# Kernel tuning notes

Measured on AMD Instinct MI355X. Metric: run time of the kernel, lower is better.

## Reference

```python
import jax, jax.numpy as jnp
import numpy as np

K = 3          # conv kernel size
PW = 4         # parallel window (pw_height == pw_width)
OC = 128       # out_channels
IC = 128       # in_channels
RANK = 256
STRIDE = PW - K + 1  # 2


def _sdk_weight_map(kernel):
    # kernel: [O, C, K, K] numpy. Concat all (top,left) zero-pad placements into PWxPW.
    O, C, k, _ = kernel.shape
    d = PW - k
    maps = []
    for top in range(d + 1):
        for left in range(d + 1):
            pk = np.zeros((O, C, PW, PW), dtype=kernel.dtype)
            pk[:, :, top:top + k, left:left + k] = kernel
            maps.append(pk.reshape(O, -1))
    return np.concatenate(maps, axis=0)  # [(d+1)^2 * O, C*PW*PW]


def setup_inputs() -> dict:
    rng = np.random.default_rng(0)
    kernel = (rng.standard_normal((OC, IC, K, K)) * 0.05).astype(np.float32)
    W = _sdk_weight_map(kernel)  # [512, 2048]
    u, s, vh = np.linalg.svd(W, full_matrices=False)
    Q = (u[:, :RANK] * s[:RANK]).astype(np.float32)   # u_t @ diag(s_t)
    R = vh[:RANK].astype(np.float32)
    key = jax.random.key(0)
    x = jax.random.normal(key, (32, 128, 64, 64), dtype=jnp.float32)
    return {"x": x, "Q": jnp.asarray(Q), "R": jnp.asarray(R)}


def _slice_and_forward(x, Q, R):
    N, C, H, Wd = x.shape
    s = STRIDE
    pad_v = (H + 2 - PW) % s
    pad_h = (Wd + 2 - PW) % s
    ov = -(-(H + 2 - PW) // s) + 1   # ceil div + 1 (matches math.ceil(...)+1)
    oh = -(-(Wd + 2 - PW) // s) + 1
    xp = jnp.pad(x, ((0, 0), (0, 0), (1, 1 + pad_v), (1, 1 + pad_h)))
    # im2col / unfold: feature layout C slowest, then (i, j) within window -> matches F.unfold
    wins = [xp[:, :, i:i + s * (ov - 1) + 1:s, j:j + s * (oh - 1) + 1:s]
            for i in range(PW) for j in range(PW)]
    patches = jnp.stack(wins, axis=2)                      # [N, C, PW*PW, ov, oh]
    flat = patches.reshape(N, C * PW * PW, ov * oh).transpose(0, 2, 1)  # [N, L, C*PW*PW]
    # F.linear(flat, Q @ R) == (flat @ R^T) @ Q^T  (apply low-rank factors sequentially)
    lin = jnp.einsum('nlr,mr->nlm', jnp.einsum('nlf,rf->nlr', flat, R), Q)  # [N, L, s*s*OC]
    lin = lin.reshape(N, ov, oh, s, s, OC).transpose(0, 1, 3, 2, 4, 5)
    lin = lin.reshape(N, H + pad_v // 2, Wd + pad_h // 2, OC)
    lin = lin.transpose(0, 3, 1, 2)                        # NHWC -> NCHW
    return lin[:, :, :H, :Wd]


def reference(x, Q, R):
    return _slice_and_forward(x, Q, R)
```

## Files before the change

### kernel.cpp

```cpp
#include <hip/hip_runtime.h>
#include <hip/hip_bf16.h>

typedef __attribute__((ext_vector_type(8))) short short8;
typedef __attribute__((ext_vector_type(4))) float f32x4;
typedef unsigned int uint;
typedef __attribute__((ext_vector_type(4))) uint uint4v;

#define AS1 __attribute__((address_space(1)))
#define AS3 __attribute__((address_space(3)))

#define QB_OFF  (1u << 20)
#define XPH_OFF (1310720u)

__device__ __forceinline__ uint bf16r(float f) {
    uint u = __float_as_uint(f);
    u += 0x7FFFu + ((u >> 16) & 1u);
    return u >> 16;
}
__device__ __forceinline__ uint pk2(float lo, float hi) {
    return bf16r(lo) | (bf16r(hi) << 16);
}

__global__ __launch_bounds__(256) void prep_kernel(
    const float* __restrict__ x, const float* __restrict__ Q, const float* __restrict__ R,
    char* __restrict__ Rp4, char* __restrict__ Qp4, char* __restrict__ xph)
{
    const int bid = blockIdx.x, tid = threadIdx.x;
    if (bid < 2048) {
        __shared__ float xt[128 * 65];
        const int n = bid >> 6, h = bid & 63;
        {
            const int c = tid >> 1, half = tid & 1;
            const float4* src = (const float4*)(x + (((size_t)(n * 128 + c) * 64 + h) * 64 + half * 32));
            #pragma unroll
            for (int q = 0; q < 8; ++q) {
                float4 v = src[q];
                float* d = &xt[c * 65 + half * 32 + q * 4];
                d[0] = v.x; d[1] = v.y; d[2] = v.z; d[3] = v.w;
            }
        }
        __syncthreads();
        {
            const int w = tid >> 2, cq = tid & 3;
            uint pw[16];
            #pragma unroll
            for (int m = 0; m < 16; ++m)
                pw[m] = pk2(xt[(cq * 32 + 2 * m) * 65 + w], xt[(cq * 32 + 2 * m + 1) * 65 + w]);
            char* dst = xph + (size_t)n * 1115136 + (size_t)(h + 1) * 16896 + (w + 1) * 256 + cq * 64;
            #pragma unroll
            for (int i = 0; i < 4; ++i) {
                uint4v q4 = { pw[4 * i], pw[4 * i + 1], pw[4 * i + 2], pw[4 * i + 3] };
                *(uint4v*)(dst + i * 16) = q4;
            }
        }
        if (tid < 32) {
            int side = tid >> 4, e = tid & 15;
            uint4v z = {0, 0, 0, 0};
            *(uint4v*)(xph + (size_t)n * 1115136 + (size_t)(h + 1) * 16896 + side * 65 * 256 + e * 16) = z;
        }
        if (h == 0) {
            uint4v z = {0, 0, 0, 0};
            #pragma unroll
            for (int it = 0; it < 9; ++it) {
                int idx = tid + it * 256;
                if (idx < 2112) {
                    int rr = (idx >= 1056) ? 65 : 0;
                    int jj = idx - (rr ? 1056 : 0);
                    int col = jj >> 4, e = jj & 15;
                    *(uint4v*)(xph + (size_t)n * 1115136 + (size_t)rr * 16896 + col * 256 + e * 16) = z;
                }
            }
        }
    } else if (bid < 2304) {
        int g = (bid - 2048) * 256 + tid;
        int kgp = g & 3, col = (g >> 2) & 255, ks = g >> 10;
        const float* src = R + (size_t)col * 2048 + ((ks & 3) * 32 + kgp * 8) * 16 + (ks >> 2);
        uint pw[4];
        #pragma unroll
        for (int m = 0; m < 4; ++m)
            pw[m] = pk2(src[(2 * m) * 16], src[(2 * m + 1) * 16]);
        uint4v q4 = { pw[0], pw[1], pw[2], pw[3] };
        int dst = ks * 16384 + (col >> 6) * 4096 + ((col >> 4) & 3) * 1024 + (kgp * 16 + (col & 15)) * 16;
        *(uint4v*)(Rp4 + dst) = q4;
    } else {
        int g = (bid - 2304) * 256 + tid;
        int kgp = g & 3, col = (g >> 2) & 511, ks = g >> 11;
        const float4* s = (const float4*)(Q + (size_t)col * 256 + ks * 32 + kgp * 8);
        float4 a = s[0], b = s[1];
        uint4v q4 = { pk2(a.x, a.y), pk2(a.z, a.w), pk2(b.x, b.y), pk2(b.z, b.w) };
        int dst = ks * 32768 + (col >> 7) * 8192 + ((col >> 4) & 7) * 1024 + (kgp * 16 + (col & 15)) * 16;
        *(uint4v*)(Qp4 + dst) = q4;
    }
}

__global__ __launch_bounds__(256, 2) void fused_kernel(
    const char* __restrict__ xph, const char* __restrict__ Rp4,
    const char* __restrict__ Qp4, float* __restrict__ out)
{
    extern __shared__ __align__(16) char lds[];

    const int b0 = blockIdx.x;
    const int b = (b0 & 7) * 64 + (b0 >> 3);
    const int n = b >> 4, vt = b & 15;
    const int tid = threadIdx.x;
    const int wave = tid >> 6, lane = tid & 63;
    const int lr = lane & 15, kg = lane >> 4;
    const int lr7 = lr & 7;

    const char* xbase = xph + (size_t)n * 1115136;

    int xconst[4], xw[4];
    #pragma unroll
    for (int q = 0; q < 4; ++q) {
        int p = (q * 4 + wave) * 64 + lane;
        int rh = p >> 9, cl = (p >> 4) & 31, sl = p & 15;
        xconst[q] = (vt * 4 + 2 * rh) * 16896 + (2 * cl) * 256 + ((sl ^ (cl & 7)) << 4);
        xw[q] = p * 16;
    }
    int abase[4];
    #pragma unroll
    for (int mf = 0; mf < 4; ++mf) {
        int m = mf * 16 + lr;
        abase[mf] = (m >> 5) * 8192 + (m & 31) * 256;
    }
    const char* Rw = Rp4 + wave * 4096 + lane * 16;
    const char* Qw = Qp4 + wave * 8192 + lane * 16;

    f32x4 acc[4][4];
    #pragma unroll
    for (int i = 0; i < 4; ++i)
        #pragma unroll
        for (int j = 0; j < 4; ++j) acc[i][j] = (f32x4)0.f;

    short8 bfA[16], bfB[16];

#define XSTAGE(sp_) if ((sp_) < 16) { int i1_ = (sp_) >> 2, j1_ = (sp_) & 3;           \
        int xb_ = ((sp_) % 3) * 16384;                                                 \
        _Pragma("unroll") for (int q = 0; q < 4; ++q)                                  \
            __builtin_amdgcn_global_load_lds(                                          \
                (const AS1 void*)(xbase + xconst[q] + i1_ * 16896 + j1_ * 256),        \
                (AS3 void*)(lds + xb_ + xw[q]), 16, 0, 0); }

#define BLOAD16(dst_, kG_) if ((kG_) < 16) {                                           \
        _Pragma("unroll") for (int u = 0; u < 4; ++u)                                  \
            _Pragma("unroll") for (int nf = 0; nf < 4; ++nf)                           \
                dst_[u * 4 + nf] = *(const short8*)(Rw + (size_t)(4 * (kG_) + u) * 16384 + nf * 1024); }

#define MFMAG(bf_, xb_) {                                                              \
        _Pragma("unroll") for (int u = 0; u < 4; ++u) {                                \
            short8 af[4];                                                              \
            _Pragma("unroll") for (int mf = 0; mf < 4; ++mf)                           \
                af[mf] = *(const short8*)(lds + (xb_) + abase[mf] + (((u * 4 + kg) ^ lr7) << 4)); \
            _Pragma("unroll") for (int nf = 0; nf < 4; ++nf)                           \
                _Pragma("unroll") for (int mf = 0; mf < 4; ++mf)                       \
                    acc[mf][nf] = __builtin_amdgcn_mfma_f32_16x16x32_bf16(af[mf], bf_[u * 4 + nf], acc[mf][nf], 0, 0, 0); } }

#define BAR(Nstr) { __builtin_amdgcn_sched_barrier(0);                                 \
        asm volatile("s_waitcnt vmcnt(" Nstr ") lgkmcnt(0)\n\ts_barrier" ::: "memory");\
        __builtin_amdgcn_sched_barrier(0); }

    BLOAD16(bfA, 0);
    XSTAGE(0); XSTAGE(1);
    __builtin_amdgcn_sched_barrier(0);
    asm volatile("s_waitcnt vmcnt(4)\n\ts_barrier" ::: "memory");
    __builtin_amdgcn_sched_barrier(0);

    for (int g = 0; g < 14; g += 2) {
        BLOAD16(bfB, g + 1);
        XSTAGE(g + 2);
        MFMAG(bfA, (g % 3) * 16384);
        BAR("20")
        BLOAD16(bfA, g + 2);
        XSTAGE(g + 3);
        MFMAG(bfB, ((g + 1) % 3) * 16384);
        BAR("20")
    }
    BLOAD16(bfB, 15);
    MFMAG(bfA, 32768);
    BAR("16")
    MFMAG(bfB, 0);

    {
        char* tt_ = lds + 49152;
        #pragma unroll
        for (int mf = 0; mf < 4; ++mf)
            #pragma unroll
            for (int nf = 0; nf < 4; ++nf)
                #pragma unroll
                for (int r = 0; r < 4; ++r) {
                    int row = mf * 16 + kg * 4 + r;
                    int col = wave * 64 + nf * 16 + lr;
                    *(ushort*)(tt_ + row * 512 + ((col * 2) ^ ((row & 7) << 4))) =
                        (ushort)bf16r(acc[mf][nf][r]);
                }
    }
    __syncthreads();

    f32x4 acc2[4][8];
    #pragma unroll
    for (int i = 0; i < 4; ++i)
        #pragma unroll
        for (int j = 0; j < 8; ++j) acc2[i][j] = (f32x4)0.f;
    {
        const char* tt_ = lds + 49152;
        #pragma unroll
        for (int ks = 0; ks < 8; ++ks) {
            short8 af2[4];
            #pragma unroll
            for (int mf = 0; mf < 4; ++mf) {
                int ml = mf * 16 + lr;
                af2[mf] = *(const short8*)(tt_ + ml * 512 + (((ks * 32 + kg * 8) * 2) ^ ((ml & 7) << 4)));
            }
            #pragma unroll
            for (int nf = 0; nf < 8; ++nf) {
                const short8 bfr = *(const short8*)(Qw + (size_t)ks * 32768 + nf * 1024);
                #pragma unroll
                for (int mf = 0; mf < 4; ++mf)
                    acc2[mf][nf] = __builtin_amdgcn_mfma_f32_16x16x32_bf16(af2[mf], bfr, acc2[mf][nf], 0, 0, 0);
            }
        }
    }

    float* ep = (float*)lds;
    const int si_w = wave >> 1, sj_w = wave & 1;
    #pragma unroll
    for (int si_p = 0; si_p < 2; ++si_p)
        #pragma unroll
        for (int vl_p = 0; vl_p < 2; ++vl_p) {
            __syncthreads();
            if (si_w == si_p) {
                #pragma unroll
                for (int mfh = 0; mfh < 2; ++mfh) {
                    int mf = vl_p * 2 + mfh;
                    #pragma unroll
                    for (int nf = 0; nf < 8; ++nf)
                        #pragma unroll
                        for (int r = 0; r < 4; ++r) {
                            int row_l = mfh * 16 + kg * 4 + r;
                            int col = sj_w * 128 + nf * 16 + lr;
                            ep[row_l * 257 + col] = acc2[mf][nf][r];
                        }
                }
            }
            __syncthreads();
            const int r_out = (vt * 2 + vl_p) * 2 + si_p;
            float* obase = out + (size_t)n * 524288 + (size_t)r_out * 64;
            #pragma unroll
            for (int it = 0; it < 32; ++it) {
                int idx = tid + it * 256;
                int cc = idx & 63, oc = idx >> 6;
                obase[(size_t)oc * 4096 + cc] = ep[(cc >> 1) * 257 + (cc & 1) * 128 + oc];
            }
        }
}

extern "C" void kernel_launch(void* const* d_in, const int* in_sizes, int n_in,
                              void* d_out, int out_size, void* d_ws, size_t ws_size,
                              hipStream_t stream) {
    const float* x = (const float*)d_in[0];
    const float* Q = (const float*)d_in[1];
    const float* R = (const float*)d_in[2];
    float* out = (float*)d_out;

    char* ws = (char*)d_ws;
    char* Rp4 = ws;
    char* Qp4 = ws + QB_OFF;
    char* xph = ws + XPH_OFF;

    prep_kernel<<<2368, 256, 0, stream>>>(x, Q, R, Rp4, Qp4, xph);
    fused_kernel<<<512, 256, 81920, stream>>>(xph, Rp4, Qp4, out);
}
```

Baseline: 77.07 us.

## Double M tile to 128 rows with 8 waves and stream R/Q through LDS

The fused kernel now uses 512-thread blocks that each own 128 output positions instead of 64, with a 2x4 wave grid, which halves the grid and doubles reuse of the R and Q weights per block. R and Q are staged into LDS with async global_load_lds double buffering instead of being loaded per wave into registers, and the prep kernel relayouts them to match. The epilogue writes float4 vectorized, swizzled output rows. The block needs 128KB of LDS and halves the number of blocks, which limits occupancy and risks lower CU utilization with only 256 blocks.

```diff
diff --git a/kernel.cpp b/kernel.cpp
--- a/kernel.cpp
+++ b/kernel.cpp
@@ -73,58 +73,86 @@
         }
     } else if (bid < 2304) {
         int g = (bid - 2048) * 256 + tid;
-        int kgp = g & 3, col = (g >> 2) & 255, ks = g >> 10;
-        const float* src = R + (size_t)col * 2048 + ((ks & 3) * 32 + kgp * 8) * 16 + (ks >> 2);
+        int hg = g >> 11, p = g & 2047;
+        int col = p >> 3;
+        int kgx = (p & 7) ^ (col & 7);
+        const float* src = R + (size_t)col * 2048 + (((hg & 1) * 64 + kgx * 8) * 16 + (hg >> 1));
         uint pw[4];
         #pragma unroll
         for (int m = 0; m < 4; ++m)
             pw[m] = pk2(src[(2 * m) * 16], src[(2 * m + 1) * 16]);
         uint4v q4 = { pw[0], pw[1], pw[2], pw[3] };
-        int dst = ks * 16384 + (col >> 6) * 4096 + ((col >> 4) & 3) * 1024 + (kgp * 16 + (col & 15)) * 16;
-        *(uint4v*)(Rp4 + dst) = q4;
+        *(uint4v*)(Rp4 + (size_t)hg * 32768 + p * 16) = q4;
     } else {
         int g = (bid - 2304) * 256 + tid;
-        int kgp = g & 3, col = (g >> 2) & 511, ks = g >> 11;
-        const float4* s = (const float4*)(Q + (size_t)col * 256 + ks * 32 + kgp * 8);
+        int ks = g >> 11, p = g & 2047;
+        int col = p >> 2, unit = p & 3;
+        const float4* s = (const float4*)(Q + (size_t)col * 256 + ks * 32 + unit * 8);
         float4 a = s[0], b = s[1];
         uint4v q4 = { pk2(a.x, a.y), pk2(a.z, a.w), pk2(b.x, b.y), pk2(b.z, b.w) };
-        int dst = ks * 32768 + (col >> 7) * 8192 + ((col >> 4) & 7) * 1024 + (kgp * 16 + (col & 15)) * 16;
-        *(uint4v*)(Qp4 + dst) = q4;
-    }
-}
-
-__global__ __launch_bounds__(256, 2) void fused_kernel(
+        *(uint4v*)(Qp4 + (size_t)ks * 32768 + p * 16) = q4;
+    }
+}
+
+__global__ __launch_bounds__(512, 2) void fused_kernel(
     const char* __restrict__ xph, const char* __restrict__ Rp4,
     const char* __restrict__ Qp4, float* __restrict__ out)
 {
     extern __shared__ __align__(16) char lds[];
 
     const int b0 = blockIdx.x;
-    const int b = (b0 & 7) * 64 + (b0 >> 3);
-    const int n = b >> 4, vt = b & 15;
+    const int b = (b0 & 7) * 32 + (b0 >> 3);
+    const int n = b >> 3, vt = b & 7;
     const int tid = threadIdx.x;
     const int wave = tid >> 6, lane = tid & 63;
     const int lr = lane & 15, kg = lane >> 4;
     const int lr7 = lr & 7;
+    const int wm = wave >> 2, wn = wave & 3;
 
     const char* xbase = xph + (size_t)n * 1115136;
 
-    int xconst[4], xw[4];
+    int pdst[4], xoff[4];
     #pragma unroll
     for (int q = 0; q < 4; ++q) {
-        int p = (q * 4 + wave) * 64 + lane;
-        int rh = p >> 9, cl = (p >> 4) & 31, sl = p & 15;
-        xconst[q] = (vt * 4 + 2 * rh) * 16896 + (2 * cl) * 256 + ((sl ^ (cl & 7)) << 4);
-        xw[q] = p * 16;
-    }
-    int abase[4];
+        int p = q * 512 + tid;
+        pdst[q] = p * 16;
+        int m = p >> 4, sl = p & 15;
+        xoff[q] = (8 * vt + 2 * (m >> 5)) * 16896 + (2 * (m & 31)) * 256 + ((sl ^ (m & 7)) << 4);
+    }
+    int abase[4], tbase[4];
     #pragma unroll
     for (int mf = 0; mf < 4; ++mf) {
-        int m = mf * 16 + lr;
-        abase[mf] = (m >> 5) * 8192 + (m & 31) * 256;
-    }
-    const char* Rw = Rp4 + wave * 4096 + lane * 16;
-    const char* Qw = Qp4 + wave * 8192 + lane * 16;
+        int m = wm * 64 + mf * 16 + lr;
+        abase[mf] = m * 256;
+        tbase[mf] = m * 512;
+    }
+    int bbase[4];
+    #pragma unroll
+    for (int nf = 0; nf < 4; ++nf) bbase[nf] = (wn * 64 + nf * 16 + lr) * 128;
+    int qbase[8];
+    #pragma unroll
+    for (int nf = 0; nf < 8; ++nf)
+        qbase[nf] = ((wn >> 1) * 256 + (nf >> 2) * 128 + (wn & 1) * 64 + (nf & 3) * 16 + lr) * 64;
+
+#define BDMA(hg_, sb_) { _Pragma("unroll") for (int q = 0; q < 4; ++q)                  \
+        __builtin_amdgcn_global_load_lds(                                               \
+            (const AS1 void*)(Rp4 + (size_t)(hg_) * 32768 + pdst[q]),                   \
+            (AS3 void*)(lds + 65536 + (sb_) * 32768 + pdst[q]), 16, 0, 0); }
+#define XDMA(g_, sx_) { _Pragma("unroll") for (int q = 0; q < 4; ++q)                   \
+        __builtin_amdgcn_global_load_lds(                                               \
+            (const AS1 void*)(xbase + xoff[q] + ((g_) >> 2) * 16896 + ((g_) & 3) * 256),\
+            (AS3 void*)(lds + (sx_) * 32768 + pdst[q]), 16, 0, 0); }
+#define QDMA(ks_, sq_) { _Pragma("unroll") for (int q = 0; q < 4; ++q)                  \
+        __builtin_amdgcn_global_load_lds(                                               \
+            (const AS1 void*)(Qp4 + (size_t)(ks_) * 32768 + pdst[q]),                   \
+            (AS3 void*)(lds + 65536 + (sq_) * 32768 + pdst[q]), 16, 0, 0); }
+
+#define BAR(Nstr) { __builtin_amdgcn_sched_barrier(0);                                  \
+        asm volatile("s_waitcnt vmcnt(" Nstr ") lgkmcnt(0)\n\ts_barrier" ::: "memory"); \
+        __builtin_amdgcn_sched_barrier(0); }
+#define LBAR { __builtin_amdgcn_sched_barrier(0);                                       \
+        asm volatile("s_waitcnt lgkmcnt(0)\n\ts_barrier" ::: "memory");                 \
+        __builtin_amdgcn_sched_barrier(0); }
 
     f32x4 acc[4][4];
     #pragma unroll
@@ -132,126 +160,103 @@
         #pragma unroll
         for (int j = 0; j < 4; ++j) acc[i][j] = (f32x4)0.f;
 
-    short8 bfA[16], bfB[16];
-
-#define XSTAGE(sp_) if ((sp_) < 16) { int i1_ = (sp_) >> 2, j1_ = (sp_) & 3;           \
-        int xb_ = ((sp_) % 3) * 16384;                                                 \
-        _Pragma("unroll") for (int q = 0; q < 4; ++q)                                  \
-            __builtin_amdgcn_global_load_lds(                                          \
-                (const AS1 void*)(xbase + xconst[q] + i1_ * 16896 + j1_ * 256),        \
-                (AS3 void*)(lds + xb_ + xw[q]), 16, 0, 0); }
-
-#define BLOAD16(dst_, kG_) if ((kG_) < 16) {                                           \
-        _Pragma("unroll") for (int u = 0; u < 4; ++u)                                  \
-            _Pragma("unroll") for (int nf = 0; nf < 4; ++nf)                           \
-                dst_[u * 4 + nf] = *(const short8*)(Rw + (size_t)(4 * (kG_) + u) * 16384 + nf * 1024); }
-
-#define MFMAG(bf_, xb_) {                                                              \
-        _Pragma("unroll") for (int u = 0; u < 4; ++u) {                                \
-            short8 af[4];                                                              \
-            _Pragma("unroll") for (int mf = 0; mf < 4; ++mf)                           \
-                af[mf] = *(const short8*)(lds + (xb_) + abase[mf] + (((u * 4 + kg) ^ lr7) << 4)); \
-            _Pragma("unroll") for (int nf = 0; nf < 4; ++nf)                           \
-                _Pragma("unroll") for (int mf = 0; mf < 4; ++mf)                       \
-                    acc[mf][nf] = __builtin_amdgcn_mfma_f32_16x16x32_bf16(af[mf], bf_[u * 4 + nf], acc[mf][nf], 0, 0, 0); } }
-
-#define BAR(Nstr) { __builtin_amdgcn_sched_barrier(0);                                 \
-        asm volatile("s_waitcnt vmcnt(" Nstr ") lgkmcnt(0)\n\ts_barrier" ::: "memory");\
-        __builtin_amdgcn_sched_barrier(0); }
-
-    BLOAD16(bfA, 0);
-    XSTAGE(0); XSTAGE(1);
+    BDMA(0, 0); XDMA(0, 0); BDMA(1, 1); XDMA(1, 1);
     __builtin_amdgcn_sched_barrier(0);
-    asm volatile("s_waitcnt vmcnt(4)\n\ts_barrier" ::: "memory");
+    asm volatile("s_waitcnt vmcnt(8)\n\ts_barrier" ::: "memory");
     __builtin_amdgcn_sched_barrier(0);
 
-    for (int g = 0; g < 14; g += 2) {
-        BLOAD16(bfB, g + 1);
-        XSTAGE(g + 2);
-        MFMAG(bfA, (g % 3) * 16384);
-        BAR("20")
-        BLOAD16(bfA, g + 2);
-        XSTAGE(g + 3);
-        MFMAG(bfB, ((g + 1) % 3) * 16384);
-        BAR("20")
-    }
-    BLOAD16(bfB, 15);
-    MFMAG(bfA, 32768);
-    BAR("16")
-    MFMAG(bfB, 0);
-
-    {
-        char* tt_ = lds + 49152;
-        #pragma unroll
-        for (int mf = 0; mf < 4; ++mf)
+    #pragma unroll
+    for (int h = 0; h < 32; ++h) {
+        if (h >= 1 && h <= 30) BDMA(h + 1, (h + 1) & 1);
+        if ((h & 1) == 0 && h >= 2 && h <= 28) XDMA((h >> 1) + 1, ((h >> 1) + 1) & 1);
+        if (h == 31) QDMA(0, 0);
+        const char* xs = lds + ((h >> 1) & 1) * 32768;
+        const char* bs = lds + 65536 + (h & 1) * 32768;
+        #pragma unroll
+        for (int u = 0; u < 2; ++u) {
+            const int ug = (h & 1) * 2 + u;
+            short8 af[4], bf[4];
+            #pragma unroll
+            for (int mf = 0; mf < 4; ++mf)
+                af[mf] = *(const short8*)(xs + abase[mf] + (((ug * 4 + kg) ^ lr7) << 4));
+            #pragma unroll
+            for (int nf = 0; nf < 4; ++nf)
+                bf[nf] = *(const short8*)(bs + bbase[nf] + (((u * 4 + kg) ^ lr7) << 4));
             #pragma unroll
             for (int nf = 0; nf < 4; ++nf)
                 #pragma unroll
-                for (int r = 0; r < 4; ++r) {
-                    int row = mf * 16 + kg * 4 + r;
-                    int col = wave * 64 + nf * 16 + lr;
-                    *(ushort*)(tt_ + row * 512 + ((col * 2) ^ ((row & 7) << 4))) =
-                        (ushort)bf16r(acc[mf][nf][r]);
+                for (int mf = 0; mf < 4; ++mf)
+                    acc[mf][nf] = __builtin_amdgcn_mfma_f32_16x16x32_bf16(af[mf], bf[nf], acc[mf][nf], 0, 0, 0);
+        }
+        if ((h & 1) == 0 && h <= 28) { BAR("4") } else { BAR("0") }
+    }
+
+    #pragma unroll
+    for (int mf = 0; mf < 4; ++mf)
+        #pragma unroll
+        for (int nf = 0; nf < 4; ++nf)
+            #pragma unroll
+            for (int r = 0; r < 4; ++r) {
+                int row = wm * 64 + mf * 16 + kg * 4 + r;
+                int col = wn * 64 + nf * 16 + lr;
+                *(ushort*)(lds + row * 512 + ((col * 2) ^ ((row & 7) << 4))) =
+                    (ushort)bf16r(acc[mf][nf][r]);
+            }
+    QDMA(1, 1);
+    LBAR
+
+    f32x4 acc2[4][8];
+    #pragma unroll
+    for (int i = 0; i < 4; ++i)
+        #pragma unroll
+        for (int j = 0; j < 8; ++j) acc2[i][j] = (f32x4)0.f;
+    #pragma unroll
+    for (int ks = 0; ks < 8; ++ks) {
+        if (ks >= 1 && ks <= 6) QDMA(ks + 1, (ks + 1) & 1);
+        const char* qs = lds + 65536 + (ks & 1) * 32768;
+        short8 af2[4];
+        #pragma unroll
+        for (int mf = 0; mf < 4; ++mf)
+            af2[mf] = *(const short8*)(lds + tbase[mf] + (((ks * 32 + kg * 8) * 2) ^ (lr7 << 4)));
+        #pragma unroll
+        for (int nf = 0; nf < 8; ++nf) {
+            const short8 bq = *(const short8*)(qs + qbase[nf] + (kg << 4));
+            #pragma unroll
+            for (int mf = 0; mf < 4; ++mf)
+                acc2[mf][nf] = __builtin_amdgcn_mfma_f32_16x16x32_bf16(af2[mf], bq, acc2[mf][nf], 0, 0, 0);
+        }
+        BAR("0")
+    }
+
+    const int si = wn >> 1, ochalf = wn & 1;
+    #pragma unroll
+    for (int mh = 0; mh < 4; ++mh) {
+        LBAR
+        if (wm == (mh >> 1)) {
+            #pragma unroll
+            for (int mfh = 0; mfh < 2; ++mfh) {
+                const int mf = (mh & 1) * 2 + mfh;
+                #pragma unroll
+                for (int q = 0; q < 4; ++q) {
+                    const int oc = ochalf * 64 + q * 16 + lr;
+                    const int ub = si * 34816 + oc * 272 + (((4 * mfh + kg) ^ (oc & 7)) << 5);
+                    f32x4 v0 = { acc2[mf][q][0], acc2[mf][4 + q][0], acc2[mf][q][1], acc2[mf][4 + q][1] };
+                    f32x4 v1 = { acc2[mf][q][2], acc2[mf][4 + q][2], acc2[mf][q][3], acc2[mf][4 + q][3] };
+                    *(f32x4*)(lds + ub) = v0;
+                    *(f32x4*)(lds + ub + 16) = v1;
                 }
-    }
-    __syncthreads();
-
-    f32x4 acc2[4][8];
-    #pragma unroll
-    for (int i = 0; i < 4; ++i)
-        #pragma unroll
-        for (int j = 0; j < 8; ++j) acc2[i][j] = (f32x4)0.f;
-    {
-        const char* tt_ = lds + 49152;
-        #pragma unroll
-        for (int ks = 0; ks < 8; ++ks) {
-            short8 af2[4];
-            #pragma unroll
-            for (int mf = 0; mf < 4; ++mf) {
-                int ml = mf * 16 + lr;
-                af2[mf] = *(const short8*)(tt_ + ml * 512 + (((ks * 32 + kg * 8) * 2) ^ ((ml & 7) << 4)));
-            }
-            #pragma unroll
-            for (int nf = 0; nf < 8; ++nf) {
-                const short8 bfr = *(const short8*)(Qw + (size_t)ks * 32768 + nf * 1024);
-                #pragma unroll
-                for (int mf = 0; mf < 4; ++mf)
-                    acc2[mf][nf] = __builtin_amdgcn_mfma_f32_16x16x32_bf16(af2[mf], bfr, acc2[mf][nf], 0, 0, 0);
-            }
-        }
-    }
-
-    float* ep = (float*)lds;
-    const int si_w = wave >> 1, sj_w = wave & 1;
-    #pragma unroll
-    for (int si_p = 0; si_p < 2; ++si_p)
-        #pragma unroll
-        for (int vl_p = 0; vl_p < 2; ++vl_p) {
-            __syncthreads();
-            if (si_w == si_p) {
-                #pragma unroll
-                for (int mfh = 0; mfh < 2; ++mfh) {
-                    int mf = vl_p * 2 + mfh;
-                    #pragma unroll
-                    for (int nf = 0; nf < 8; ++nf)
-                        #pragma unroll
-                        for (int r = 0; r < 4; ++r) {
-                            int row_l = mfh * 16 + kg * 4 + r;
-                            int col = sj_w * 128 + nf * 16 + lr;
-                            ep[row_l * 257 + col] = acc2[mf][nf][r];
-                        }
-                }
-            }
-            __syncthreads();
-            const int r_out = (vt * 2 + vl_p) * 2 + si_p;
-            float* obase = out + (size_t)n * 524288 + (size_t)r_out * 64;
-            #pragma unroll
-            for (int it = 0; it < 32; ++it) {
-                int idx = tid + it * 256;
-                int cc = idx & 63, oc = idx >> 6;
-                obase[(size_t)oc * 4096 + cc] = ep[(cc >> 1) * 257 + (cc & 1) * 128 + oc];
-            }
-        }
+            }
+        }
+        LBAR
+        #pragma unroll
+        for (int it = 0; it < 8; ++it) {
+            int uidx = it * 512 + tid;
+            int w4 = uidx & 15, oc = (uidx >> 4) & 127, sie = uidx >> 11;
+            f32x4 v = *(const f32x4*)(lds + sie * 34816 + oc * 272 + ((w4 ^ (2 * (oc & 7))) << 4));
+            *(f32x4*)(out + (size_t)n * 524288 + (size_t)oc * 4096
+                          + (8 * vt + 2 * mh + sie) * 64 + w4 * 4) = v;
+        }
+    }
 }
 
 extern "C" void kernel_launch(void* const* d_in, const int* in_sizes, int n_in,
@@ -268,5 +273,5 @@
     char* xph = ws + XPH_OFF;
 
     prep_kernel<<<2368, 256, 0, stream>>>(x, Q, R, Rp4, Qp4, xph);
-    fused_kernel<<<512, 256, 81920, stream>>>(xph, Rp4, Qp4, out);
-}
+    fused_kernel<<<256, 512, 131072, stream>>>(xph, Rp4, Qp4, out);
+}
```

Result: no change. 77.64 us (+0.7%).
